# Optimization experiments

Measured on AMD Instinct MI355X. Metric: run time of the kernel, lower is better.

Reference implementation:

```python
import jax, jax.numpy as jnp
import numpy as np
import math

CS = 8       # cell_size
NBINS = 8
SIGMA = 1.0
IMG = 224
BATCH = 256
TWO_PI = 2.0 * math.pi


def setup_inputs() -> dict:
    key = jax.random.key(0)
    x = jax.random.normal(key, (BATCH, 3, IMG, IMG), dtype=jnp.float32)
    coords = jnp.arange(CS, dtype=jnp.float32) - (CS - 1) / 2.0
    xx, yy = jnp.meshgrid(coords, coords, indexing='ij')
    gauss = jnp.exp(-(xx ** 2 + yy ** 2) / (2.0 * SIGMA ** 2)).reshape(1, CS * CS)
    kx = jnp.array([[-1., 0., 1.], [-2., 0., 2.], [-1., 0., 1.]], dtype=jnp.float32).reshape(1, 1, 3, 3)
    ky = jnp.array([[-1., -2., -1.], [0., 0., 0.], [1., 2., 1.]], dtype=jnp.float32).reshape(1, 1, 3, 3)
    return {"x": x, "gauss": gauss, "kx": kx, "ky": ky}


def _conv(im, k):
    # NCHW conv, padding=1, stride=1 (matches F.conv2d(..., padding=1))
    return jax.lax.conv_general_dilated(
        im, k, window_strides=(1, 1), padding=[(1, 1), (1, 1)],
        dimension_numbers=('NCHW', 'OIHW', 'NCHW'))


def reference(x, gauss, kx, ky):
    bs, _, H, W = x.shape
    gray = 0.2989 * x[:, 0:1] + 0.587 * x[:, 1:2] + 0.114 * x[:, 2:3]  # [bs,1,H,W]
    gx = _conv(gray, kx)
    gy = _conv(gray, ky)
    mag = jnp.sqrt(gx ** 2 + gy ** 2 + 1e-6)
    ang = jnp.mod(jnp.arctan2(gy, gx), TWO_PI)
    Hc, Wc = H // CS, W // CS
    n_cells = Hc * Wc

    def to_cells(a):
        # [bs,1,H,W] -> [bs*n_cells, CS*CS], within-cell order (kh,kw) row-major
        # matching F.unfold's kernel-position ordering.
        return a.reshape(bs, Hc, CS, Wc, CS).transpose(0, 1, 3, 2, 4).reshape(bs * n_cells, CS * CS)

    mags = to_cells(mag) * gauss  # gauss broadcasts over kernel positions
    angs = to_cells(ang)

    bin_w = TWO_PI / NBINS
    idx = (angs / bin_w).astype(jnp.int32) % NBINS  # [bs*n_cells, CS*CS]

    N = bs * n_cells
    hist = jnp.zeros((N, NBINS), dtype=mags.dtype)
    hist = hist.at[jnp.arange(N)[:, None], idx].add(mags)  # scatter_add per cell
    hist = hist.reshape(bs, n_cells * NBINS)
    hist = hist / (jnp.linalg.norm(hist, axis=1, keepdims=True) + 1e-6)
    return hist
```

## Files before the change

kernel.cpp:

```cpp
#include <hip/hip_runtime.h>
#include <math.h>

#define NBINS 8
#define IMG 224
#define HC 28
#define OUTPER (HC*HC*NBINS)
#define BATCH 256
#define PL (IMG*IMG)

__device__ __forceinline__ float dpp_swap1(float x) {
    return __int_as_float(__builtin_amdgcn_update_dpp(
        0, __float_as_int(x), 0xB1, 0xF, 0xF, false));
}

template<bool EDGE>
__device__ __forceinline__ void load_gray(const float* __restrict__ xb,
                                          int r0, int col4, int lane,
                                          float4 v[10])
{
    #pragma unroll
    for (int j = 0; j < 10; ++j) {
        int gr  = r0 - 1 + j;
        int grc = EDGE ? (gr < 0 ? 0 : (gr > IMG - 1 ? IMG - 1 : gr)) : gr;
        const float* p = xb + grc * IMG + col4;
        float4 R = *(const float4*)(p);
        float4 G = *(const float4*)(p + PL);
        float4 B = *(const float4*)(p + 2 * PL);
        float4 g;
        g.x = 0.2989f * R.x + 0.587f * G.x + 0.114f * B.x;
        g.y = 0.2989f * R.y + 0.587f * G.y + 0.114f * B.y;
        g.z = 0.2989f * R.z + 0.587f * G.z + 0.114f * B.z;
        g.w = 0.2989f * R.w + 0.587f * G.w + 0.114f * B.w;
        bool z = (lane >= 56) || (EDGE && (gr < 0 || gr > IMG - 1));
        if (z) { g.x = 0.f; g.y = 0.f; g.z = 0.f; g.w = 0.f; }
        v[j] = g;
    }
}

__global__ __launch_bounds__(256) void hog_main_kernel(
    const float* __restrict__ x, const float* __restrict__ gauss,
    float* __restrict__ out, float* __restrict__ partial)
{
    const int tid  = threadIdx.x;
    const int wv   = tid >> 6;
    const int lane = tid & 63;
    const int bc   = blockIdx.x;
    const int b    = bc / 7;
    const int cr   = (bc - b * 7) * 4 + wv;
    const int r0   = cr * 8;
    const int li   = lane < 55 ? lane : 55;
    const int col4 = li * 4;

    const float* xb = x + (size_t)b * 3 * PL;

    float4 v[10];
    if (cr == 0 || cr == HC - 1) load_gray<true >(xb, r0, col4, lane, v);
    else                         load_gray<false>(xb, r0, col4, lane, v);

    const float E0 = 0.0021874911f, E1 = 0.043936934f,
                E2 = 0.32465247f,   E3 = 0.88249690f;
    const bool odd = (lane & 1);
    const float ew0 = odd ? E3 : E0, ew1 = odd ? E2 : E1,
                ew2 = odd ? E1 : E2, ew3 = odd ? E0 : E3;
    const float EROW[8] = { E0, E1, E2, E3, E3, E2, E1, E0 };

    float h[8];
    #pragma unroll
    for (int k = 0; k < 8; ++k) h[k] = 0.f;

    auto pix = [&](float gx, float gy, float w) {
        float mag = __builtin_amdgcn_sqrtf(gx * gx + gy * gy + 1e-6f);
        float ax = fabsf(gx), ay = fabsf(gy);
        int bin;
        if (gy > 0.f)       bin = (gx > 0.f)  ? ((gy < gx) ? 0 : 1)
                                : (gx == 0.f) ? 2 : ((ay > ax) ? 2 : 3);
        else if (gy == 0.f) bin = (gx < 0.f) ? 4 : 0;
        else                bin = (gx < 0.f)  ? ((ay < ax) ? 4 : 5)
                                : (gx == 0.f) ? 6 : ((ay > ax) ? 6 : 7);
        float wm = w * mag;
        #pragma unroll
        for (int k = 0; k < 8; ++k) h[k] += (bin == k) ? wm : 0.f;
    };

    #pragma unroll
    for (int sr = 0; sr < 8; ++sr) {
        float4 t = v[sr], m = v[sr + 1], bt = v[sr + 2];
        float4 s, d;
        s.x = t.x + 2.f * m.x + bt.x;  s.y = t.y + 2.f * m.y + bt.y;
        s.z = t.z + 2.f * m.z + bt.z;  s.w = t.w + 2.f * m.w + bt.w;
        d.x = bt.x - t.x;  d.y = bt.y - t.y;
        d.z = bt.z - t.z;  d.w = bt.w - t.w;

        float sL = __shfl_up(s.w, 1, 64);   sL = (lane == 0) ? 0.f : sL;
        float dL = __shfl_up(d.w, 1, 64);   dL = (lane == 0) ? 0.f : dL;
        float sR = __shfl_down(s.x, 1, 64);
        float dR = __shfl_down(d.x, 1, 64);

        float gx0 = s.y - sL,  gx1 = s.z - s.x,
              gx2 = s.w - s.y, gx3 = sR  - s.z;
        float gy0 = dL  + 2.f * d.x + d.y, gy1 = d.x + 2.f * d.y + d.z,
              gy2 = d.y + 2.f * d.z + d.w, gy3 = d.z + 2.f * d.w + dR;

        float er = EROW[sr];
        pix(gx0, gy0, er * ew0);
        pix(gx1, gy1, er * ew1);
        pix(gx2, gy2, er * ew2);
        pix(gx3, gy3, er * ew3);
    }

    #pragma unroll
    for (int k = 0; k < 8; ++k) h[k] += dpp_swap1(h[k]);

    float ssq = 0.f;
    if (lane < 56) {
        float4 st = odd ? make_float4(h[4], h[5], h[6], h[7])
                        : make_float4(h[0], h[1], h[2], h[3]);
        *(float4*)(out + (size_t)b * OUTPER + (size_t)cr * IMG + 4 * lane) = st;
        ssq = st.x * st.x + st.y * st.y + st.z * st.z + st.w * st.w;
    }

    #pragma unroll
    for (int o = 32; o > 0; o >>= 1) ssq += __shfl_down(ssq, o, 64);
    if (lane == 0) partial[b * HC + cr] = ssq;
}

__global__ __launch_bounds__(256) void hog_norm_kernel(
    float* __restrict__ out, const float* __restrict__ partial)
{
    const int bq = blockIdx.x, tid = threadIdx.x;
    const int b = bq >> 2, q = bq & 3;
    __shared__ float wsum[4];
    __shared__ float s_inv;
    float s = (tid < HC) ? partial[b * HC + tid] : 0.f;
    #pragma unroll
    for (int o = 32; o > 0; o >>= 1) s += __shfl_down(s, o, 64);
    if ((tid & 63) == 0) wsum[tid >> 6] = s;
    __syncthreads();
    if (tid == 0) {
        float t = wsum[0] + wsum[1] + wsum[2] + wsum[3];
        s_inv = 1.0f / (sqrtf(t) + 1e-6f);
    }
    __syncthreads();
    float inv = s_inv;
    float4* o4 = (float4*)(out + (size_t)b * OUTPER + (size_t)q * (OUTPER / 4));
    for (int i = tid; i < OUTPER / 16; i += 256) {
        float4 w = o4[i];
        w.x *= inv; w.y *= inv; w.z *= inv; w.w *= inv;
        o4[i] = w;
    }
}

extern "C" void kernel_launch(void* const* d_in, const int* in_sizes, int n_in,
                              void* d_out, int out_size, void* d_ws, size_t ws_size,
                              hipStream_t stream) {
    const float* x     = (const float*)d_in[0];
    const float* gauss = (const float*)d_in[1];
    float* out     = (float*)d_out;
    float* partial = (float*)d_ws;

    hog_main_kernel<<<BATCH * 7, 256, 0, stream>>>(x, gauss, out, partial);
    hog_norm_kernel<<<BATCH * 4, 256, 0, stream>>>(out, partial);
}
```

Baseline: 230.8 us.

## Stage grayscale band in LDS to share halo rows across waves

Each block now cooperatively loads a 34-row grayscale band into shared memory once, with zero-padded column borders, instead of each wave loading its own 10 rows from global memory. That removes the 2-row halo overlap between the four waves. Lateral neighbours for the Sobel stencil are read from LDS, replacing cross-lane shuffles. In exchange it adds a block-wide barrier and about 31 KB of LDS per block, which may limit occupancy.

```diff
diff --git a/kernel.cpp b/kernel.cpp
--- a/kernel.cpp
+++ b/kernel.cpp
@@ -7,55 +7,69 @@
 #define OUTPER (HC*HC*NBINS)
 #define BATCH 256
 #define PL (IMG*IMG)
+#define BANDR 34
+#define LDSW 232
+#define NF4 (BANDR*56)
 
 __device__ __forceinline__ float dpp_swap1(float x) {
     return __int_as_float(__builtin_amdgcn_update_dpp(
         0, __float_as_int(x), 0xB1, 0xF, 0xF, false));
 }
 
-template<bool EDGE>
-__device__ __forceinline__ void load_gray(const float* __restrict__ xb,
-                                          int r0, int col4, int lane,
-                                          float4 v[10])
-{
-    #pragma unroll
-    for (int j = 0; j < 10; ++j) {
-        int gr  = r0 - 1 + j;
-        int grc = EDGE ? (gr < 0 ? 0 : (gr > IMG - 1 ? IMG - 1 : gr)) : gr;
-        const float* p = xb + grc * IMG + col4;
-        float4 R = *(const float4*)(p);
-        float4 G = *(const float4*)(p + PL);
-        float4 B = *(const float4*)(p + 2 * PL);
-        float4 g;
-        g.x = 0.2989f * R.x + 0.587f * G.x + 0.114f * B.x;
-        g.y = 0.2989f * R.y + 0.587f * G.y + 0.114f * B.y;
-        g.z = 0.2989f * R.z + 0.587f * G.z + 0.114f * B.z;
-        g.w = 0.2989f * R.w + 0.587f * G.w + 0.114f * B.w;
-        bool z = (lane >= 56) || (EDGE && (gr < 0 || gr > IMG - 1));
-        if (z) { g.x = 0.f; g.y = 0.f; g.z = 0.f; g.w = 0.f; }
-        v[j] = g;
-    }
-}
-
 __global__ __launch_bounds__(256) void hog_main_kernel(
     const float* __restrict__ x, const float* __restrict__ gauss,
     float* __restrict__ out, float* __restrict__ partial)
 {
-    const int tid  = threadIdx.x;
+    __shared__ float gs[BANDR * LDSW];
+
+    const int tid = threadIdx.x;
+    const int bc  = blockIdx.x;
+    const int b   = bc / 7;
+    const int blk = bc - b * 7;
+    const int rowTop = blk * 32 - 1;
+    const float* xb = x + (size_t)b * 3 * PL;
+
+    if (tid < 2 * BANDR) {
+        int r = tid >> 1;
+        gs[r * LDSW + ((tid & 1) ? 228 : 3)] = 0.f;
+    }
+
+    auto fill_one = [&](int i) {
+        int r    = i / 56;
+        int c4   = (i - r * 56) * 4;
+        int grow = rowTop + r;
+        int gc   = grow < 0 ? 0 : (grow > IMG - 1 ? IMG - 1 : grow);
+        const float* p = xb + gc * IMG + c4;
+        float4 R = *(const float4*)(p);
+        float4 G = *(const float4*)(p + PL);
+        float4 B = *(const float4*)(p + 2 * PL);
+        bool z = (grow != gc);
+        float4 g;
+        g.x = z ? 0.f : 0.2989f * R.x + 0.587f * G.x + 0.114f * B.x;
+        g.y = z ? 0.f : 0.2989f * R.y + 0.587f * G.y + 0.114f * B.y;
+        g.z = z ? 0.f : 0.2989f * R.z + 0.587f * G.z + 0.114f * B.z;
+        g.w = z ? 0.f : 0.2989f * R.w + 0.587f * G.w + 0.114f * B.w;
+        *(float4*)&gs[r * LDSW + c4 + 4] = g;
+    };
+    #pragma unroll
+    for (int it = 0; it < 7; ++it) fill_one(tid + it * 256);
+    if (tid < NF4 - 7 * 256) fill_one(tid + 7 * 256);
+
+    __syncthreads();
+
     const int wv   = tid >> 6;
     const int lane = tid & 63;
-    const int bc   = blockIdx.x;
-    const int b    = bc / 7;
-    const int cr   = (bc - b * 7) * 4 + wv;
-    const int r0   = cr * 8;
+    const int cr   = blk * 4 + wv;
     const int li   = lane < 55 ? lane : 55;
-    const int col4 = li * 4;
 
-    const float* xb = x + (size_t)b * 3 * PL;
-
-    float4 v[10];
-    if (cr == 0 || cr == HC - 1) load_gray<true >(xb, r0, col4, lane, v);
-    else                         load_gray<false>(xb, r0, col4, lane, v);
+    float4 v[10]; float hl[10], hr[10];
+    const float* base = gs + (wv * 8) * LDSW + li * 4 + 4;
+    #pragma unroll
+    for (int j = 0; j < 10; ++j) {
+        v[j]  = *(const float4*)(base + j * LDSW);
+        hl[j] = base[j * LDSW - 1];
+        hr[j] = base[j * LDSW + 4];
+    }
 
     const float E0 = 0.0021874911f, E1 = 0.043936934f,
                 E2 = 0.32465247f,   E3 = 0.88249690f;
@@ -85,21 +99,22 @@
     #pragma unroll
     for (int sr = 0; sr < 8; ++sr) {
         float4 t = v[sr], m = v[sr + 1], bt = v[sr + 2];
-        float4 s, d;
-        s.x = t.x + 2.f * m.x + bt.x;  s.y = t.y + 2.f * m.y + bt.y;
-        s.z = t.z + 2.f * m.z + bt.z;  s.w = t.w + 2.f * m.w + bt.w;
-        d.x = bt.x - t.x;  d.y = bt.y - t.y;
-        d.z = bt.z - t.z;  d.w = bt.w - t.w;
+        float tl = hl[sr], ml = hl[sr + 1], bl = hl[sr + 2];
+        float tr = hr[sr], mr = hr[sr + 1], br = hr[sr + 2];
+        float sm1 = tl  + 2.f * ml  + bl;
+        float s0  = t.x + 2.f * m.x + bt.x;
+        float s1  = t.y + 2.f * m.y + bt.y;
+        float s2  = t.z + 2.f * m.z + bt.z;
+        float s3  = t.w + 2.f * m.w + bt.w;
+        float s4  = tr  + 2.f * mr  + br;
+        float dm1 = bl  - tl;
+        float d0  = bt.x - t.x, d1 = bt.y - t.y,
+              d2  = bt.z - t.z, d3 = bt.w - t.w;
+        float d4  = br - tr;
 
-        float sL = __shfl_up(s.w, 1, 64);   sL = (lane == 0) ? 0.f : sL;
-        float dL = __shfl_up(d.w, 1, 64);   dL = (lane == 0) ? 0.f : dL;
-        float sR = __shfl_down(s.x, 1, 64);
-        float dR = __shfl_down(d.x, 1, 64);
-
-        float gx0 = s.y - sL,  gx1 = s.z - s.x,
-              gx2 = s.w - s.y, gx3 = sR  - s.z;
-        float gy0 = dL  + 2.f * d.x + d.y, gy1 = d.x + 2.f * d.y + d.z,
-              gy2 = d.y + 2.f * d.z + d.w, gy3 = d.z + 2.f * d.w + dR;
+        float gx0 = s1 - sm1, gx1 = s2 - s0, gx2 = s3 - s1, gx3 = s4 - s2;
+        float gy0 = dm1 + 2.f * d0 + d1, gy1 = d0 + 2.f * d1 + d2,
+              gy2 = d1  + 2.f * d2 + d3, gy3 = d2 + 2.f * d3 + d4;
 
         float er = EROW[sr];
         pix(gx0, gy0, er * ew0);
```

After: 248.1 us. 7.5% more time.
